# Kernel tuning notes

Measured on AMD Instinct MI355X. Metric: run time of the kernel, lower is better.

The kernel has to match this reference:

```python
import jax, jax.numpy as jnp
import numpy as np

LN_EPS = 1e-5
NORM_EPS = 1e-12  # F.normalize eps


def _l2norm(x):
    # torch F.normalize(p=2, dim=-1): x / max(||x||, eps)
    n = jnp.sqrt(jnp.sum(x * x, axis=-1, keepdims=True))
    return x / jnp.maximum(n, NORM_EPS)


def setup_inputs() -> dict:
    key = jax.random.key(0)
    D, R, H = 256, 32, 64  # d_model, rank, d_model//4
    B, C, P = 32, 64, 96
    ks = jax.random.split(key, 16)
    s = 0.05
    return {
        "x": jax.random.normal(ks[0], (B * C, P, D), jnp.float32),
        "ln_gamma": jnp.ones((D,), jnp.float32),
        "ln_beta": jnp.zeros((D,), jnp.float32),
        "Wd": jax.random.normal(ks[1], (D, R), jnp.float32) * s,
        "bd": jax.random.normal(ks[2], (R,), jnp.float32) * s,
        "Wq": jax.random.normal(ks[3], (R, R), jnp.float32) * s,
        "Wk": jax.random.normal(ks[4], (R, R), jnp.float32) * s,
        "Wv": jax.random.normal(ks[5], (R, R), jnp.float32) * s,
        "Wg": jax.random.normal(ks[6], (R, R), jnp.float32) * s,
        "bg": jax.random.normal(ks[7], (R,), jnp.float32) * s,
        "Wu": jax.random.normal(ks[8], (R, D), jnp.float32) * s,
        "bu": jax.random.normal(ks[9], (D,), jnp.float32) * s,
        "W1": jax.random.normal(ks[10], (D, H), jnp.float32) * s,
        "b1": jax.random.normal(ks[11], (H,), jnp.float32) * s,
        "W2": jax.random.normal(ks[12], (H, D), jnp.float32) * s,
        "b2": jnp.full((D,), -5.0, jnp.float32),  # gate_init bias
        "B": B,
        "C": C,
    }


def reference(x, ln_gamma, ln_beta, Wd, bd, Wq, Wk, Wv, Wg, bg, Wu, bu, W1, b1, W2, b2, B, C):
    BC, P, D = x.shape
    # [B*C, P, D] -> [B*P, C, D] channel-mixing layout
    h = x.reshape(B, C, P, D).transpose(0, 2, 1, 3).reshape(B * P, C, D)

    # LayerNorm over D (biased variance, as in torch LayerNorm)
    mu = jnp.mean(h, axis=-1, keepdims=True)
    var = jnp.var(h, axis=-1, keepdims=True)
    h_norm = (h - mu) * jax.lax.rsqrt(var + LN_EPS) * ln_gamma + ln_beta

    # bottleneck projection to rank R
    h_low = h_norm @ Wd + bd  # [BP, C, R]

    # Hydra linear attention: cosine-normalized Q/K, sum-pooled K*V global feature
    Q = _l2norm(h_low @ Wq)
    K = _l2norm(h_low @ Wk)
    V = h_low @ Wv
    global_feat = jnp.sum(K * V, axis=1, keepdims=True)  # [BP, 1, R]
    h_attn = Q * global_feat

    # content gate and up-projection
    gate_c = jax.nn.sigmoid(h_low @ Wg + bg)
    mixed = (h_attn * gate_c) @ Wu + bu  # [BP, C, D]

    # AdaptiveGate: unbiased variance over channel dim (torch .var default ddof=1)
    chan_var = jnp.var(h, axis=1, ddof=1)  # [BP, D]
    gate_logits = jax.nn.gelu(chan_var @ W1 + b1, approximate=False) @ W2 + b2
    gate = jax.nn.sigmoid(gate_logits)[:, None, :]  # [BP, 1, D]

    out = h + gate * mixed
    # back to [B*C, P, D]
    return out.reshape(B, P, C, D).transpose(0, 2, 1, 3).reshape(BC, P, D)
```

## Files before the change

kernel.cpp:

```cpp
#include <hip/hip_runtime.h>
#include <hip/hip_bf16.h>

#define DD 256
#define RR 32
#define CC 64
#define PB 96
#define NT 512

typedef __attribute__((ext_vector_type(8))) short short8;
typedef __attribute__((ext_vector_type(4))) float f32x4;

__device__ __forceinline__ short f2bf(float f) {
    return __builtin_bit_cast(short, __float2bfloat16(f));
}
__device__ __forceinline__ float b2f(unsigned short s) {
    union { unsigned u; float f; } v; v.u = ((unsigned)s) << 16;
    return v.f;
}

__device__ __forceinline__ int hswz(int c, int d) {
    return c * 256 + (d ^ ((c & 7) << 3));
}
__device__ __forceinline__ int nswz(int r, int k) {
    return r * 32 + (k ^ (((r >> 1) & 3) << 3));
}

__global__ __launch_bounds__(1024, 1)
void prep_kernel(const float* __restrict__ ln_g, const float* __restrict__ ln_b,
                 const float* __restrict__ Wd, const float* __restrict__ bd,
                 const float* __restrict__ Wq, const float* __restrict__ Wk,
                 const float* __restrict__ Wv, const float* __restrict__ Wg,
                 const float* __restrict__ Wu,
                 short* __restrict__ wsF1, short* __restrict__ wsF2,
                 short* __restrict__ wsF3, float* __restrict__ wsLN)
{
    __shared__ float redp[2048];
    const int t = threadIdx.x;
    {
        const int r = t >> 5, dblk = t & 31;
        float sa = 0.f, sb = 0.f;
        #pragma unroll
        for (int j = 0; j < 8; ++j) {
            const int d = dblk * 8 + j;
            const float wd = Wd[d * RR + r];
            sa += ln_g[d] * wd;
            sb += ln_b[d] * wd;
        }
        redp[r * 32 + dblk]        = sa;
        redp[1024 + r * 32 + dblk] = sb;
    }
    {
        const int f = t >> 6, l = t & 63;
        const int rt = f >> 3, step = f & 7;
        const int r = rt * 16 + (l & 15);
        short8 v;
        #pragma unroll
        for (int j = 0; j < 8; ++j) {
            const int d = step * 32 + (l >> 4) * 8 + j;
            v[j] = f2bf(ln_g[d] * Wd[d * RR + r]);
        }
        *(short8*)&wsF1[f * 512 + l * 8] = v;
    }
    if (t < 512) {
        const int f = t >> 6, l = t & 63;
        const int m = f >> 1, half = f & 1;
        const float* Wm = (m == 0) ? Wq : (m == 1) ? Wk : (m == 2) ? Wv : Wg;
        const int rout = half * 16 + (l & 15);
        short8 v;
        #pragma unroll
        for (int j = 0; j < 8; ++j) {
            const int rin = (l >> 4) * 8 + j;
            v[j] = f2bf(Wm[rin * RR + rout]);
        }
        *(short8*)&wsF2[f * 512 + l * 8] = v;
    }
    {
        const int f = t >> 6, l = t & 63;
        const int d = f * 16 + (l & 15);
        short8 v;
        #pragma unroll
        for (int j = 0; j < 8; ++j) {
            const int r = (l >> 4) * 8 + j;
            v[j] = f2bf(Wu[r * DD + d]);
        }
        *(short8*)&wsF3[f * 512 + l * 8] = v;
    }
    __syncthreads();
    if (t < 32) {
        float s = 0.f;
        #pragma unroll
        for (int g = 0; g < 32; ++g) s += redp[t * 32 + g];
        wsLN[t] = s;
    } else if (t < 64) {
        const int r = t - 32;
        float s = 0.f;
        #pragma unroll
        for (int g = 0; g < 32; ++g) s += redp[1024 + r * 32 + g];
        wsLN[t] = s + bd[r];
    }
}

__global__ __launch_bounds__(NT, 6)
void hydra_kernel(const float* __restrict__ x,
                  const short* __restrict__ wsF1, const short* __restrict__ wsF2,
                  const short* __restrict__ wsF3, const float* __restrict__ wsLN,
                  const float* __restrict__ bg, const float* __restrict__ bu,
                  const float* __restrict__ W1, const float* __restrict__ b1,
                  const float* __restrict__ W2, const float* __restrict__ b2,
                  float* __restrict__ out)
{
    __shared__ short hbf[CC * DD];
    __shared__ float pool_f[1024];
    __shared__ float redA[128];
    __shared__ float cv_s[DD];
    __shared__ float gate_s[DD];
    __shared__ float mu_s[CC], rstd_s[CC];
    __shared__ float hid_s[64];
    __shared__ float ln_a[RR], ln_bv[RR];

    short* qg   = hbf;
    short* hlow = hbf + 2048;
    short* Abuf = (short*)pool_f;

    const int t    = threadIdx.x;
    const int lane = t & 63;
    const int w    = t >> 6;
    const int bp   = blockIdx.x;
    const int b    = bp / PB;
    const int p    = bp - b * PB;
    const size_t rowbase = (size_t)(b * CC) * PB * DD + (size_t)p * DD;

    #pragma unroll
    for (int i = 0; i < 8; ++i) {
        const int c = w * 8 + i;
        const float4 v = *(const float4*)(x + rowbase + (size_t)c * (PB * DD) + 4 * lane);
        float s1 = v.x + v.y + v.z + v.w;
        float s2 = v.x * v.x + v.y * v.y + v.z * v.z + v.w * v.w;
        s1 += __shfl_xor(s1, 1, 64); s2 += __shfl_xor(s2, 1, 64);
        s1 += __shfl_xor(s1, 2, 64); s2 += __shfl_xor(s2, 2, 64);
        s1 += __shfl_xor(s1, 4, 64); s2 += __shfl_xor(s2, 4, 64);
        s1 += __shfl_xor(s1, 8, 64); s2 += __shfl_xor(s2, 8, 64);
        if ((lane & 15) == 0)
            *(float2*)&pool_f[(c * 4 + (lane >> 4)) * 2] = make_float2(s1, s2);
        ushort4 pk;
        pk.x = (unsigned short)f2bf(v.x); pk.y = (unsigned short)f2bf(v.y);
        pk.z = (unsigned short)f2bf(v.z); pk.w = (unsigned short)f2bf(v.w);
        *(ushort4*)&hbf[hswz(c, 4 * lane)] = pk;
    }
    if (t < 32)            ln_a[t]       = wsLN[t];
    else if (t < 64)       ln_bv[t - 32] = wsLN[t];
    __syncthreads();

    f32x4 acc0 = {0.f,0.f,0.f,0.f}, acc1 = {0.f,0.f,0.f,0.f};
    if (w < 4) {
        const int ct = w;
        if (lane < 16) {
            const int c = ct * 16 + lane;
            const float2 p0 = *(const float2*)&pool_f[(c * 4 + 0) * 2];
            const float2 p1 = *(const float2*)&pool_f[(c * 4 + 1) * 2];
            const float2 p2 = *(const float2*)&pool_f[(c * 4 + 2) * 2];
            const float2 p3 = *(const float2*)&pool_f[(c * 4 + 3) * 2];
            const float s1 = p0.x + p1.x + p2.x + p3.x;
            const float s2 = p0.y + p1.y + p2.y + p3.y;
            const float mu = s1 * (1.f / 256.f);
            mu_s[c]   = mu;
            rstd_s[c] = rsqrtf(s2 * (1.f / 256.f) - mu * mu + 1e-5f);
        }
        const int arow = ct * 16 + (lane & 15);
        const int kofs = (lane >> 4) * 8;
        #pragma unroll
        for (int step = 0; step < 8; ++step) {
            const short8 a   = *(const short8*)&hbf[hswz(arow, step * 32 + kofs)];
            const short8 bf0 = *(const short8*)(wsF1 + step * 512 + lane * 8);
            const short8 bf1 = *(const short8*)(wsF1 + (8 + step) * 512 + lane * 8);
            acc0 = __builtin_amdgcn_mfma_f32_16x16x32_bf16(a, bf0, acc0, 0, 0, 0);
            acc1 = __builtin_amdgcn_mfma_f32_16x16x32_bf16(a, bf1, acc1, 0, 0, 0);
        }
    } else {
        const int d = t - 256;
        float s1 = 0.f, s2 = 0.f;
        #pragma unroll 8
        for (int c = 0; c < CC; ++c) {
            const float v = b2f((unsigned short)hbf[hswz(c, d)]);
            s1 += v; s2 += v * v;
        }
        cv_s[d] = (s2 - s1 * s1 * (1.f / 64.f)) * (1.f / 63.f);
    }
    __syncthreads();

    if (w < 4) {
        const int ct = w;
        const int col0 = lane & 15, col1 = 16 + col0;
        {
            const float la0 = ln_a[col0], lb0 = ln_bv[col0];
            const float la1 = ln_a[col1], lb1 = ln_bv[col1];
            #pragma unroll
            for (int i = 0; i < 4; ++i) {
                const int c = ct * 16 + (lane >> 4) * 4 + i;
                const float rs = rstd_s[c], mu = mu_s[c];
                hlow[nswz(c, col0)] = f2bf(rs * acc0[i] - rs * mu * la0 + lb0);
                hlow[nswz(c, col1)] = f2bf(rs * acc1[i] - rs * mu * la1 + lb1);
            }
        }
        const int arow = ct * 16 + col0;
        const int kofs = (lane >> 4) * 8;
        const short8 a = *(const short8*)&hlow[nswz(arow, kofs)];
        const short8 bQ0 = *(const short8*)(wsF2 + 0 * 512 + lane * 8);
        const short8 bQ1 = *(const short8*)(wsF2 + 1 * 512 + lane * 8);
        const short8 bK0 = *(const short8*)(wsF2 + 2 * 512 + lane * 8);
        const short8 bK1 = *(const short8*)(wsF2 + 3 * 512 + lane * 8);
        const short8 bV0 = *(const short8*)(wsF2 + 4 * 512 + lane * 8);
        const short8 bV1 = *(const short8*)(wsF2 + 5 * 512 + lane * 8);
        const short8 bG0 = *(const short8*)(wsF2 + 6 * 512 + lane * 8);
        const short8 bG1 = *(const short8*)(wsF2 + 7 * 512 + lane * 8);
        f32x4 aQ0={0,0,0,0}, aQ1={0,0,0,0}, aK0={0,0,0,0}, aK1={0,0,0,0};
        f32x4 aV0={0,0,0,0}, aV1={0,0,0,0}, aG0={0,0,0,0}, aG1={0,0,0,0};
        aQ0 = __builtin_amdgcn_mfma_f32_16x16x32_bf16(a, bQ0, aQ0, 0, 0, 0);
        aQ1 = __builtin_amdgcn_mfma_f32_16x16x32_bf16(a, bQ1, aQ1, 0, 0, 0);
        aK0 = __builtin_amdgcn_mfma_f32_16x16x32_bf16(a, bK0, aK0, 0, 0, 0);
        aK1 = __builtin_amdgcn_mfma_f32_16x16x32_bf16(a, bK1, aK1, 0, 0, 0);
        aV0 = __builtin_amdgcn_mfma_f32_16x16x32_bf16(a, bV0, aV0, 0, 0, 0);
        aV1 = __builtin_amdgcn_mfma_f32_16x16x32_bf16(a, bV1, aV1, 0, 0, 0);
        aG0 = __builtin_amdgcn_mfma_f32_16x16x32_bf16(a, bG0, aG0, 0, 0, 0);
        aG1 = __builtin_amdgcn_mfma_f32_16x16x32_bf16(a, bG1, aG1, 0, 0, 0);
        float qs[4], ks[4];
        #pragma unroll
        for (int i = 0; i < 4; ++i) {
            float sq = aQ0[i] * aQ0[i] + aQ1[i] * aQ1[i];
            float sk = aK0[i] * aK0[i] + aK1[i] * aK1[i];
            sq += __shfl_xor(sq, 1, 64); sk += __shfl_xor(sk, 1, 64);
            sq += __shfl_xor(sq, 2, 64); sk += __shfl_xor(sk, 2, 64);
            sq += __shfl_xor(sq, 4, 64); sk += __shfl_xor(sk, 4, 64);
            sq += __shfl_xor(sq, 8, 64); sk += __shfl_xor(sk, 8, 64);
            qs[i] = 1.f / fmaxf(sqrtf(sq), 1e-12f);
            ks[i] = 1.f / fmaxf(sqrtf(sk), 1e-12f);
        }
        const float bgv0 = bg[col0], bgv1 = bg[col1];
        float p0 = 0.f, p1 = 0.f;
        #pragma unroll
        for (int i = 0; i < 4; ++i) {
            const int c = ct * 16 + (lane >> 4) * 4 + i;
            const float g0 = 1.f / (1.f + __expf(-(aG0[i] + bgv0)));
            const float g1 = 1.f / (1.f + __expf(-(aG1[i] + bgv1)));
            qg[c * 32 + col0] = f2bf(aQ0[i] * qs[i] * g0);
            qg[c * 32 + col1] = f2bf(aQ1[i] * qs[i] * g1);
            p0 += (aK0[i] * ks[i]) * aV0[i];
            p1 += (aK1[i] * ks[i]) * aV1[i];
        }
        p0 += __shfl_xor(p0, 16, 64); p1 += __shfl_xor(p1, 16, 64);
        p0 += __shfl_xor(p0, 32, 64); p1 += __shfl_xor(p1, 32, 64);
        if (lane < 16) {
            redA[ct * 32 + lane]      = p0;
            redA[ct * 32 + 16 + lane] = p1;
        }
    } else {
        const int j = (w - 4) * 16 + (lane >> 2);
        const int q = lane & 3;
        float s = 0.f;
        #pragma unroll 8
        for (int i = 0; i < 64; ++i) {
            const int d = q * 64 + i;
            s += cv_s[d] * W1[d * 64 + j];
        }
        s += __shfl_xor(s, 1, 64);
        s += __shfl_xor(s, 2, 64);
        if (q == 0) {
            const float z = s + b1[j];
            hid_s[j] = 0.5f * z * (1.f + erff(z * 0.70710678118654752f));
        }
    }
    __syncthreads();

    if (t < 256) {
        const int r = t & 31, cb = t >> 5;
        const float gf = redA[r] + redA[32 + r] + redA[64 + r] + redA[96 + r];
        #pragma unroll
        for (int k = 0; k < 8; ++k) {
            const int c = cb * 8 + k;
            Abuf[nswz(c, r)] = f2bf(b2f((unsigned short)qg[c * 32 + r]) * gf);
        }
    } else {
        const int d = t - 256;
        float s = b2[d];
        #pragma unroll 8
        for (int j = 0; j < 64; ++j)
            s += hid_s[j] * W2[j * DD + d];
        gate_s[d] = 1.f / (1.f + __expf(-s));
    }
    __syncthreads();

    {
        const int ct = w & 3, dgh = w >> 2;
        const int arow = ct * 16 + (lane & 15);
        const int kofs = (lane >> 4) * 8;
        const short8 a = *(const short8*)&Abuf[nswz(arow, kofs)];
        #pragma unroll
        for (int j = 0; j < 8; ++j) {
            const int dt = dgh * 8 + j;
            const int col = dt * 16 + (lane & 15);
            const short8 bf = *(const short8*)(wsF3 + dt * 512 + lane * 8);
            f32x4 acc = {0.f, 0.f, 0.f, 0.f};
            acc = __builtin_amdgcn_mfma_f32_16x16x32_bf16(a, bf, acc, 0, 0, 0);
            #pragma unroll
            for (int i = 0; i < 4; ++i) {
                const int c = ct * 16 + (lane >> 4) * 4 + i;
                hbf[hswz(c, col)] = f2bf(acc[i]);
            }
        }
    }
    __syncthreads();

    #pragma unroll
    for (int i = 0; i < 8; ++i) {
        const int c = w * 8 + i;
        const size_t off = rowbase + (size_t)c * (PB * DD) + 4 * lane;
        const float4 xv = *(const float4*)(x + off);
        const ushort4 m = *(const ushort4*)&hbf[hswz(c, 4 * lane)];
        const float4 g4 = *(const float4*)&gate_s[4 * lane];
        const float4 bu4 = *(const float4*)(bu + 4 * lane);
        float4 o;
        o.x = xv.x + g4.x * (b2f(m.x) + bu4.x);
        o.y = xv.y + g4.y * (b2f(m.y) + bu4.y);
        o.z = xv.z + g4.z * (b2f(m.z) + bu4.z);
        o.w = xv.w + g4.w * (b2f(m.w) + bu4.w);
        *(float4*)(out + off) = o;
    }
}

extern "C" void kernel_launch(void* const* d_in, const int* in_sizes, int n_in,
                              void* d_out, int out_size, void* d_ws, size_t ws_size,
                              hipStream_t stream) {
    (void)in_sizes; (void)n_in; (void)out_size; (void)ws_size;
    const float* x    = (const float*)d_in[0];
    const float* ln_g = (const float*)d_in[1];
    const float* ln_b = (const float*)d_in[2];
    const float* Wd   = (const float*)d_in[3];
    const float* bd   = (const float*)d_in[4];
    const float* Wq   = (const float*)d_in[5];
    const float* Wk   = (const float*)d_in[6];
    const float* Wv   = (const float*)d_in[7];
    const float* Wg   = (const float*)d_in[8];
    const float* bg   = (const float*)d_in[9];
    const float* Wu   = (const float*)d_in[10];
    const float* bu   = (const float*)d_in[11];
    const float* W1   = (const float*)d_in[12];
    const float* b1   = (const float*)d_in[13];
    const float* W2   = (const float*)d_in[14];
    const float* b2   = (const float*)d_in[15];
    float* out = (float*)d_out;

    short* wsF1 = (short*)d_ws;
    short* wsF2 = wsF1 + 8192;
    short* wsF3 = wsF2 + 4096;
    float* wsLN = (float*)(wsF1 + 20480);

    prep_kernel<<<dim3(1), dim3(1024), 0, stream>>>(
        ln_g, ln_b, Wd, bd, Wq, Wk, Wv, Wg, Wu, wsF1, wsF2, wsF3, wsLN);
    hydra_kernel<<<dim3(32 * PB), dim3(NT), 0, stream>>>(
        x, wsF1, wsF2, wsF3, wsLN, bg, bu, W1, b1, W2, b2, out);
}
```

Measured before the change: 165.5 us.

## Fuse up-projection into epilogue, drop x reread, use 1024-thread blocks

Doubles the block to 1024 threads and stages the LN-folded Wd in LDS. Prep now writes transposed W1/W2 so the adaptive-gate matvecs use contiguous float4 loads. The final MFMA results stay in registers and are written straight to the output, using the bf16 copy of x held in LDS as the residual instead of reading x from global memory again. This removes a full second read of x and a shared-memory round trip, but costs residual precision, produces scalar, less coalesced stores, and raises LDS use per block.

After: 172.2 us. +4.0%, slower.

```diff
diff --git a/kernel.cpp b/kernel.cpp
--- a/kernel.cpp
+++ b/kernel.cpp
@@ -5,7 +5,7 @@
 #define RR 32
 #define CC 64
 #define PB 96
-#define NT 512
+#define NT 1024
 
 typedef __attribute__((ext_vector_type(8))) short short8;
 typedef __attribute__((ext_vector_type(4))) float f32x4;
@@ -31,35 +31,29 @@
                  const float* __restrict__ Wq, const float* __restrict__ Wk,
                  const float* __restrict__ Wv, const float* __restrict__ Wg,
                  const float* __restrict__ Wu,
-                 short* __restrict__ wsF1, short* __restrict__ wsF2,
-                 short* __restrict__ wsF3, float* __restrict__ wsLN)
+                 const float* __restrict__ W1, const float* __restrict__ W2,
+                 short* __restrict__ wsWd, short* __restrict__ wsF2,
+                 short* __restrict__ wsF3, float* __restrict__ wsLN,
+                 float* __restrict__ wsW1T, float* __restrict__ wsW2T)
 {
     __shared__ float redp[2048];
     const int t = threadIdx.x;
     {
         const int r = t >> 5, dblk = t & 31;
+        short8 vv;
         float sa = 0.f, sb = 0.f;
         #pragma unroll
         for (int j = 0; j < 8; ++j) {
             const int d = dblk * 8 + j;
             const float wd = Wd[d * RR + r];
-            sa += ln_g[d] * wd;
+            const float g  = ln_g[d];
+            vv[j] = f2bf(g * wd);
+            sa += g * wd;
             sb += ln_b[d] * wd;
         }
+        *(short8*)&wsWd[r * 256 + ((dblk ^ (r & 7)) << 3)] = vv;
         redp[r * 32 + dblk]        = sa;
         redp[1024 + r * 32 + dblk] = sb;
-    }
-    {
-        const int f = t >> 6, l = t & 63;
-        const int rt = f >> 3, step = f & 7;
-        const int r = rt * 16 + (l & 15);
-        short8 v;
-        #pragma unroll
-        for (int j = 0; j < 8; ++j) {
-            const int d = step * 32 + (l >> 4) * 8 + j;
-            v[j] = f2bf(ln_g[d] * Wd[d * RR + r]);
-        }
-        *(short8*)&wsF1[f * 512 + l * 8] = v;
     }
     if (t < 512) {
         const int f = t >> 6, l = t & 63;
@@ -85,6 +79,18 @@
         }
         *(short8*)&wsF3[f * 512 + l * 8] = v;
     }
+    #pragma unroll
+    for (int rep = 0; rep < 16; ++rep) {
+        const int id = rep * 1024 + t;
+        const int j = id >> 8, d = id & 255;
+        wsW1T[j * 256 + d] = W1[d * 64 + j];
+    }
+    #pragma unroll
+    for (int rep = 0; rep < 16; ++rep) {
+        const int id = rep * 1024 + t;
+        const int d = id >> 6, j = id & 63;
+        wsW2T[d * 64 + j] = W2[j * 256 + d];
+    }
     __syncthreads();
     if (t < 32) {
         float s = 0.f;
@@ -100,27 +106,25 @@
     }
 }
 
-__global__ __launch_bounds__(NT, 6)
+__global__ __launch_bounds__(NT, 8)
 void hydra_kernel(const float* __restrict__ x,
-                  const short* __restrict__ wsF1, const short* __restrict__ wsF2,
+                  const short* __restrict__ wsWd, const short* __restrict__ wsF2,
                   const short* __restrict__ wsF3, const float* __restrict__ wsLN,
+                  const float* __restrict__ wsW1T, const float* __restrict__ wsW2T,
                   const float* __restrict__ bg, const float* __restrict__ bu,
-                  const float* __restrict__ W1, const float* __restrict__ b1,
-                  const float* __restrict__ W2, const float* __restrict__ b2,
+                  const float* __restrict__ b1, const float* __restrict__ b2,
                   float* __restrict__ out)
 {
     __shared__ short hbf[CC * DD];
-    __shared__ float pool_f[1024];
-    __shared__ float redA[128];
-    __shared__ float cv_s[DD];
-    __shared__ float gate_s[DD];
+    __shared__ short wreg[RR * DD];
+    __shared__ short qg[CC * RR];
+    __shared__ short lowbuf[CC * RR];
+    __shared__ float redA[1024];
+    __shared__ float gfp[128];
+    __shared__ float cv_s[DD], gate_s[DD];
     __shared__ float mu_s[CC], rstd_s[CC];
     __shared__ float hid_s[64];
     __shared__ float ln_a[RR], ln_bv[RR];
-
-    short* qg   = hbf;
-    short* hlow = hbf + 2048;
-    short* Abuf = (short*)pool_f;
 
     const int t    = threadIdx.x;
     const int lane = t & 63;
@@ -131,66 +135,52 @@
     const size_t rowbase = (size_t)(b * CC) * PB * DD + (size_t)p * DD;
 
     #pragma unroll
-    for (int i = 0; i < 8; ++i) {
-        const int c = w * 8 + i;
+    for (int i = 0; i < 4; ++i) {
+        const int c = w * 4 + i;
         const float4 v = *(const float4*)(x + rowbase + (size_t)c * (PB * DD) + 4 * lane);
         float s1 = v.x + v.y + v.z + v.w;
         float s2 = v.x * v.x + v.y * v.y + v.z * v.z + v.w * v.w;
         s1 += __shfl_xor(s1, 1, 64); s2 += __shfl_xor(s2, 1, 64);
         s1 += __shfl_xor(s1, 2, 64); s2 += __shfl_xor(s2, 2, 64);
         s1 += __shfl_xor(s1, 4, 64); s2 += __shfl_xor(s2, 4, 64);
-        s1 += __shfl_xor(s1, 8, 64); s2 += __shfl_xor(s2, 8, 64);
-        if ((lane & 15) == 0)
-            *(float2*)&pool_f[(c * 4 + (lane >> 4)) * 2] = make_float2(s1, s2);
+        if ((lane & 7) == 0)
+            *(float2*)&redA[(c * 8 + (lane >> 3)) * 2] = make_float2(s1, s2);
         ushort4 pk;
         pk.x = (unsigned short)f2bf(v.x); pk.y = (unsigned short)f2bf(v.y);
         pk.z = (unsigned short)f2bf(v.z); pk.w = (unsigned short)f2bf(v.w);
         *(ushort4*)&hbf[hswz(c, 4 * lane)] = pk;
     }
-    if (t < 32)            ln_a[t]       = wsLN[t];
-    else if (t < 64)       ln_bv[t - 32] = wsLN[t];
-    __syncthreads();
-
-    f32x4 acc0 = {0.f,0.f,0.f,0.f}, acc1 = {0.f,0.f,0.f,0.f};
+    *(short8*)&wreg[t * 8] = *(const short8*)&wsWd[t * 8];
+    if (t < 32)              ln_a[t]       = wsLN[t];
+    else if (t < 64)         ln_bv[t - 32] = wsLN[t];
+    __syncthreads();
+
     if (w < 4) {
         const int ct = w;
         if (lane < 16) {
             const int c = ct * 16 + lane;
-            const float2 p0 = *(const float2*)&pool_f[(c * 4 + 0) * 2];
-            const float2 p1 = *(const float2*)&pool_f[(c * 4 + 1) * 2];
-            const float2 p2 = *(const float2*)&pool_f[(c * 4 + 2) * 2];
-            const float2 p3 = *(const float2*)&pool_f[(c * 4 + 3) * 2];
-            const float s1 = p0.x + p1.x + p2.x + p3.x;
-            const float s2 = p0.y + p1.y + p2.y + p3.y;
+            float s1 = 0.f, s2 = 0.f;
+            #pragma unroll
+            for (int g = 0; g < 8; ++g) {
+                const float2 pr = *(const float2*)&redA[(c * 8 + g) * 2];
+                s1 += pr.x; s2 += pr.y;
+            }
             const float mu = s1 * (1.f / 256.f);
             mu_s[c]   = mu;
             rstd_s[c] = rsqrtf(s2 * (1.f / 256.f) - mu * mu + 1e-5f);
         }
         const int arow = ct * 16 + (lane & 15);
         const int kofs = (lane >> 4) * 8;
+        const int col0 = lane & 15, col1 = 16 + col0;
+        f32x4 s3a0 = {0,0,0,0}, s3a1 = {0,0,0,0};
         #pragma unroll
         for (int step = 0; step < 8; ++step) {
-            const short8 a   = *(const short8*)&hbf[hswz(arow, step * 32 + kofs)];
-            const short8 bf0 = *(const short8*)(wsF1 + step * 512 + lane * 8);
-            const short8 bf1 = *(const short8*)(wsF1 + (8 + step) * 512 + lane * 8);
-            acc0 = __builtin_amdgcn_mfma_f32_16x16x32_bf16(a, bf0, acc0, 0, 0, 0);
-            acc1 = __builtin_amdgcn_mfma_f32_16x16x32_bf16(a, bf1, acc1, 0, 0, 0);
-        }
-    } else {
-        const int d = t - 256;
-        float s1 = 0.f, s2 = 0.f;
-        #pragma unroll 8
-        for (int c = 0; c < CC; ++c) {
-            const float v = b2f((unsigned short)hbf[hswz(c, d)]);
-            s1 += v; s2 += v * v;
-        }
-        cv_s[d] = (s2 - s1 * s1 * (1.f / 64.f)) * (1.f / 63.f);
-    }
-    __syncthreads();
-
-    if (w < 4) {
-        const int ct = w;
-        const int col0 = lane & 15, col1 = 16 + col0;
+            const short8 a  = *(const short8*)&hbf[hswz(arow, step * 32 + kofs)];
+            const short8 b0 = *(const short8*)&wreg[hswz(col0, step * 32 + kofs)];
+            const short8 b1f= *(const short8*)&wreg[hswz(col1, step * 32 + kofs)];
+            s3a0 = __builtin_amdgcn_mfma_f32_16x16x32_bf16(a, b0, s3a0, 0, 0, 0);
+            s3a1 = __builtin_amdgcn_mfma_f32_16x16x32_bf16(a, b1f, s3a1, 0, 0, 0);
+        }
         {
             const float la0 = ln_a[col0], lb0 = ln_bv[col0];
             const float la1 = ln_a[col1], lb1 = ln_bv[col1];
@@ -198,31 +188,22 @@
             for (int i = 0; i < 4; ++i) {
                 const int c = ct * 16 + (lane >> 4) * 4 + i;
                 const float rs = rstd_s[c], mu = mu_s[c];
-                hlow[nswz(c, col0)] = f2bf(rs * acc0[i] - rs * mu * la0 + lb0);
-                hlow[nswz(c, col1)] = f2bf(rs * acc1[i] - rs * mu * la1 + lb1);
-            }
-        }
-        const int arow = ct * 16 + col0;
-        const int kofs = (lane >> 4) * 8;
-        const short8 a = *(const short8*)&hlow[nswz(arow, kofs)];
-        const short8 bQ0 = *(const short8*)(wsF2 + 0 * 512 + lane * 8);
-        const short8 bQ1 = *(const short8*)(wsF2 + 1 * 512 + lane * 8);
-        const short8 bK0 = *(const short8*)(wsF2 + 2 * 512 + lane * 8);
-        const short8 bK1 = *(const short8*)(wsF2 + 3 * 512 + lane * 8);
-        const short8 bV0 = *(const short8*)(wsF2 + 4 * 512 + lane * 8);
-        const short8 bV1 = *(const short8*)(wsF2 + 5 * 512 + lane * 8);
-        const short8 bG0 = *(const short8*)(wsF2 + 6 * 512 + lane * 8);
-        const short8 bG1 = *(const short8*)(wsF2 + 7 * 512 + lane * 8);
+                lowbuf[nswz(c, col0)] = f2bf(rs * s3a0[i] - rs * mu * la0 + lb0);
+                lowbuf[nswz(c, col1)] = f2bf(rs * s3a1[i] - rs * mu * la1 + lb1);
+            }
+        }
+        const short8 av = *(const short8*)&lowbuf[nswz(arow, kofs)];
         f32x4 aQ0={0,0,0,0}, aQ1={0,0,0,0}, aK0={0,0,0,0}, aK1={0,0,0,0};
-        f32x4 aV0={0,0,0,0}, aV1={0,0,0,0}, aG0={0,0,0,0}, aG1={0,0,0,0};
-        aQ0 = __builtin_amdgcn_mfma_f32_16x16x32_bf16(a, bQ0, aQ0, 0, 0, 0);
-        aQ1 = __builtin_amdgcn_mfma_f32_16x16x32_bf16(a, bQ1, aQ1, 0, 0, 0);
-        aK0 = __builtin_amdgcn_mfma_f32_16x16x32_bf16(a, bK0, aK0, 0, 0, 0);
-        aK1 = __builtin_amdgcn_mfma_f32_16x16x32_bf16(a, bK1, aK1, 0, 0, 0);
-        aV0 = __builtin_amdgcn_mfma_f32_16x16x32_bf16(a, bV0, aV0, 0, 0, 0);
-        aV1 = __builtin_amdgcn_mfma_f32_16x16x32_bf16(a, bV1, aV1, 0, 0, 0);
-        aG0 = __builtin_amdgcn_mfma_f32_16x16x32_bf16(a, bG0, aG0, 0, 0, 0);
-        aG1 = __builtin_amdgcn_mfma_f32_16x16x32_bf16(a, bG1, aG1, 0, 0, 0);
+        {
+            const short8 bQ0 = *(const short8*)(wsF2 + 0 * 512 + lane * 8);
+            const short8 bQ1 = *(const short8*)(wsF2 + 1 * 512 + lane * 8);
+            const short8 bK0 = *(const short8*)(wsF2 + 2 * 512 + lane * 8);
+            const short8 bK1 = *(const short8*)(wsF2 + 3 * 512 + lane * 8);
+            aQ0 = __builtin_amdgcn_mfma_f32_16x16x32_bf16(av, bQ0, aQ0, 0, 0, 0);
+            aQ1 = __builtin_amdgcn_mfma_f32_16x16x32_bf16(av, bQ1, aQ1, 0, 0, 0);
+            aK0 = __builtin_amdgcn_mfma_f32_16x16x32_bf16(av, bK0, aK0, 0, 0, 0);
+            aK1 = __builtin_amdgcn_mfma_f32_16x16x32_bf16(av, bK1, aK1, 0, 0, 0);
+        }
         float qs[4], ks[4];
         #pragma unroll
         for (int i = 0; i < 4; ++i) {
@@ -235,95 +216,119 @@
             qs[i] = 1.f / fmaxf(sqrtf(sq), 1e-12f);
             ks[i] = 1.f / fmaxf(sqrtf(sk), 1e-12f);
         }
-        const float bgv0 = bg[col0], bgv1 = bg[col1];
-        float p0 = 0.f, p1 = 0.f;
-        #pragma unroll
-        for (int i = 0; i < 4; ++i) {
-            const int c = ct * 16 + (lane >> 4) * 4 + i;
-            const float g0 = 1.f / (1.f + __expf(-(aG0[i] + bgv0)));
-            const float g1 = 1.f / (1.f + __expf(-(aG1[i] + bgv1)));
-            qg[c * 32 + col0] = f2bf(aQ0[i] * qs[i] * g0);
-            qg[c * 32 + col1] = f2bf(aQ1[i] * qs[i] * g1);
-            p0 += (aK0[i] * ks[i]) * aV0[i];
-            p1 += (aK1[i] * ks[i]) * aV1[i];
-        }
-        p0 += __shfl_xor(p0, 16, 64); p1 += __shfl_xor(p1, 16, 64);
-        p0 += __shfl_xor(p0, 32, 64); p1 += __shfl_xor(p1, 32, 64);
-        if (lane < 16) {
-            redA[ct * 32 + lane]      = p0;
-            redA[ct * 32 + 16 + lane] = p1;
-        }
-    } else {
-        const int j = (w - 4) * 16 + (lane >> 2);
-        const int q = lane & 3;
-        float s = 0.f;
+        {
+            const short8 bV0 = *(const short8*)(wsF2 + 4 * 512 + lane * 8);
+            const short8 bV1 = *(const short8*)(wsF2 + 5 * 512 + lane * 8);
+            f32x4 aV0={0,0,0,0}, aV1={0,0,0,0};
+            aV0 = __builtin_amdgcn_mfma_f32_16x16x32_bf16(av, bV0, aV0, 0, 0, 0);
+            aV1 = __builtin_amdgcn_mfma_f32_16x16x32_bf16(av, bV1, aV1, 0, 0, 0);
+            float p0 = 0.f, p1 = 0.f;
+            #pragma unroll
+            for (int i = 0; i < 4; ++i) {
+                p0 += (aK0[i] * ks[i]) * aV0[i];
+                p1 += (aK1[i] * ks[i]) * aV1[i];
+            }
+            p0 += __shfl_xor(p0, 16, 64); p1 += __shfl_xor(p1, 16, 64);
+            p0 += __shfl_xor(p0, 32, 64); p1 += __shfl_xor(p1, 32, 64);
+            if (lane < 16) {
+                gfp[ct * 32 + lane]      = p0;
+                gfp[ct * 32 + 16 + lane] = p1;
+            }
+        }
+        {
+            const short8 bG0 = *(const short8*)(wsF2 + 6 * 512 + lane * 8);
+            const short8 bG1 = *(const short8*)(wsF2 + 7 * 512 + lane * 8);
+            f32x4 aG0={0,0,0,0}, aG1={0,0,0,0};
+            aG0 = __builtin_amdgcn_mfma_f32_16x16x32_bf16(av, bG0, aG0, 0, 0, 0);
+            aG1 = __builtin_amdgcn_mfma_f32_16x16x32_bf16(av, bG1, aG1, 0, 0, 0);
+            const float bgv0 = bg[col0], bgv1 = bg[col1];
+            #pragma unroll
+            for (int i = 0; i < 4; ++i) {
+                const int c = ct * 16 + (lane >> 4) * 4 + i;
+                const float g0 = 1.f / (1.f + __expf(-(aG0[i] + bgv0)));
+                const float g1 = 1.f / (1.f + __expf(-(aG1[i] + bgv1)));
+                qg[c * 32 + col0] = f2bf(aQ0[i] * qs[i] * g0);
+                qg[c * 32 + col1] = f2bf(aQ1[i] * qs[i] * g1);
+            }
+        }
+    } else if (t >= 256 && t < 384) {
+        const int d0 = (t - 256) * 2;
+        float s1a = 0.f, s2a = 0.f, s1b = 0.f, s2b = 0.f;
         #pragma unroll 8
-        for (int i = 0; i < 64; ++i) {
-            const int d = q * 64 + i;
-            s += cv_s[d] * W1[d * 64 + j];
-        }
-        s += __shfl_xor(s, 1, 64);
-        s += __shfl_xor(s, 2, 64);
-        if (q == 0) {
-            const float z = s + b1[j];
-            hid_s[j] = 0.5f * z * (1.f + erff(z * 0.70710678118654752f));
-        }
+        for (int c = 0; c < CC; ++c) {
+            const ushort2 u = *(const ushort2*)&hbf[hswz(c, d0)];
+            const float va = b2f(u.x), vb = b2f(u.y);
+            s1a += va; s2a += va * va;
+            s1b += vb; s2b += vb * vb;
+        }
+        cv_s[d0]     = (s2a - s1a * s1a * (1.f / 64.f)) * (1.f / 63.f);
+        cv_s[d0 + 1] = (s2b - s1b * s1b * (1.f / 64.f)) * (1.f / 63.f);
     }
     __syncthreads();
 
     if (t < 256) {
         const int r = t & 31, cb = t >> 5;
-        const float gf = redA[r] + redA[32 + r] + redA[64 + r] + redA[96 + r];
+        const float gf = gfp[r] + gfp[32 + r] + gfp[64 + r] + gfp[96 + r];
         #pragma unroll
         for (int k = 0; k < 8; ++k) {
             const int c = cb * 8 + k;
-            Abuf[nswz(c, r)] = f2bf(b2f((unsigned short)qg[c * 32 + r]) * gf);
-        }
-    } else {
-        const int d = t - 256;
-        float s = b2[d];
+            lowbuf[nswz(c, r)] = f2bf(b2f((unsigned short)qg[c * 32 + r]) * gf);
+        }
+    } else if (t >= 512 && t < 576) {
+        const int j = t - 512;
+        const float* w1row = wsW1T + j * 256;
+        float s = b1[j];
         #pragma unroll 8
-        for (int j = 0; j < 64; ++j)
-            s += hid_s[j] * W2[j * DD + d];
-        gate_s[d] = 1.f / (1.f + __expf(-s));
-    }
-    __syncthreads();
-
-    {
-        const int ct = w & 3, dgh = w >> 2;
+        for (int ii = 0; ii < 64; ++ii) {
+            const float4 wv  = *(const float4*)(w1row + ii * 4);
+            const float4 cvv = *(const float4*)&cv_s[ii * 4];
+            s += cvv.x * wv.x + cvv.y * wv.y + cvv.z * wv.z + cvv.w * wv.w;
+        }
+        hid_s[j] = 0.5f * s * (1.f + erff(s * 0.70710678118654752f));
+    }
+    __syncthreads();
+
+    f32x4 s8acc[8];
+    if (w < 8) {
+        const int ct = w & 3, dg = w >> 2;
         const int arow = ct * 16 + (lane & 15);
         const int kofs = (lane >> 4) * 8;
-        const short8 a = *(const short8*)&Abuf[nswz(arow, kofs)];
-        #pragma unroll
-        for (int j = 0; j < 8; ++j) {
-            const int dt = dgh * 8 + j;
-            const int col = dt * 16 + (lane & 15);
+        const short8 a = *(const short8*)&lowbuf[nswz(arow, kofs)];
+        #pragma unroll
+        for (int j = 0; j < 8; ++j) {
+            const int dt = dg * 8 + j;
             const short8 bf = *(const short8*)(wsF3 + dt * 512 + lane * 8);
-            f32x4 acc = {0.f, 0.f, 0.f, 0.f};
-            acc = __builtin_amdgcn_mfma_f32_16x16x32_bf16(a, bf, acc, 0, 0, 0);
+            f32x4 z = {0.f, 0.f, 0.f, 0.f};
+            s8acc[j] = __builtin_amdgcn_mfma_f32_16x16x32_bf16(a, bf, z, 0, 0, 0);
+        }
+    } else if (t >= 512 && t < 768) {
+        const int d = t - 512;
+        const float* w2row = wsW2T + d * 64;
+        float s = b2[d];
+        #pragma unroll
+        for (int ii = 0; ii < 16; ++ii) {
+            const float4 wv = *(const float4*)(w2row + ii * 4);
+            const float4 hv = *(const float4*)&hid_s[ii * 4];
+            s += hv.x * wv.x + hv.y * wv.y + hv.z * wv.z + hv.w * wv.w;
+        }
+        gate_s[d] = 1.f / (1.f + __expf(-s));
+    }
+    __syncthreads();
+
+    if (w < 8) {
+        const int ct = w & 3, dg = w >> 2;
+        #pragma unroll
+        for (int j = 0; j < 8; ++j) {
+            const int col = (dg * 8 + j) * 16 + (lane & 15);
+            const float gt  = gate_s[col];
+            const float buv = bu[col];
             #pragma unroll
             for (int i = 0; i < 4; ++i) {
                 const int c = ct * 16 + (lane >> 4) * 4 + i;
-                hbf[hswz(c, col)] = f2bf(acc[i]);
-            }
-        }
-    }
-    __syncthreads();
-
-    #pragma unroll
-    for (int i = 0; i < 8; ++i) {
-        const int c = w * 8 + i;
-        const size_t off = rowbase + (size_t)c * (PB * DD) + 4 * lane;
-        const float4 xv = *(const float4*)(x + off);
-        const ushort4 m = *(const ushort4*)&hbf[hswz(c, 4 * lane)];
-        const float4 g4 = *(const float4*)&gate_s[4 * lane];
-        const float4 bu4 = *(const float4*)(bu + 4 * lane);
-        float4 o;
-        o.x = xv.x + g4.x * (b2f(m.x) + bu4.x);
-        o.y = xv.y + g4.y * (b2f(m.y) + bu4.y);
-        o.z = xv.z + g4.z * (b2f(m.z) + bu4.z);
-        o.w = xv.w + g4.w * (b2f(m.w) + bu4.w);
-        *(float4*)(out + off) = o;
+                const float xv = b2f((unsigned short)hbf[hswz(c, col)]);
+                out[rowbase + (size_t)c * (PB * DD) + col] = xv + gt * (s8acc[j][i] + buv);
+            }
+        }
     }
 }
 
@@ -349,13 +354,16 @@
     const float* b2   = (const float*)d_in[15];
     float* out = (float*)d_out;
 
-    short* wsF1 = (short*)d_ws;
-    short* wsF2 = wsF1 + 8192;
-    short* wsF3 = wsF2 + 4096;
-    float* wsLN = (float*)(wsF1 + 20480);
+    short* wsWd  = (short*)d_ws;
+    short* wsF2  = wsWd + 8192;
+    short* wsF3  = wsF2 + 4096;
+    float* wsLN  = (float*)(wsWd + 20480);
+    float* wsW1T = wsLN + 64;
+    float* wsW2T = wsW1T + 16384;
 
     prep_kernel<<<dim3(1), dim3(1024), 0, stream>>>(
-        ln_g, ln_b, Wd, bd, Wq, Wk, Wv, Wg, Wu, wsF1, wsF2, wsF3, wsLN);
+        ln_g, ln_b, Wd, bd, Wq, Wk, Wv, Wg, Wu, W1, W2,
+        wsWd, wsF2, wsF3, wsLN, wsW1T, wsW2T);
     hydra_kernel<<<dim3(32 * PB), dim3(NT), 0, stream>>>(
-        x, wsF1, wsF2, wsF3, wsLN, bg, bu, W1, b1, W2, b2, out);
-}
+        x, wsWd, wsF2, wsF3, wsLN, wsW1T, wsW2T, bg, bu, b1, b2, out);
+}
```
